# Kernel tuning notes

Hardware: AMD Instinct MI355X
Metric: run time of the kernel (lower is better)

The kernel has to match this reference:

```python
import jax, jax.numpy as jnp
import numpy as np

B, N, DOP, DM, H = 8, 2048, 256, 256, 256  # batch, n_ops==n_machines, dims


def setup_inputs() -> dict:
    key = jax.random.key(0)
    ks = jax.random.split(key, 21)
    s = 0.02
    inp = {
        "operation_features": jax.random.normal(ks[0], (B, N, DOP), jnp.float32),
        "machine_features": jax.random.normal(ks[1], (B, N, DM), jnp.float32),
        "type_match_mask": jax.random.bernoulli(ks[2], 0.3, (B, N, N)).astype(jnp.float32),
        "same_type_mask": jax.random.bernoulli(ks[3], 0.3, (B, N, N)).astype(jnp.float32),
        "oma_q_w": jax.random.normal(ks[4], (H, DM), jnp.float32) * s,
        "oma_q_b": jnp.zeros((H,), jnp.float32),
        "oma_kv_w": jax.random.normal(ks[5], (2 * H, DOP), jnp.float32) * s,
        "oma_kv_b": jnp.zeros((2 * H,), jnp.float32),
        "oma_s_w": jax.random.normal(ks[6], (1, 2 * H), jnp.float32) * s,
        "oma_s_b": jnp.zeros((1,), jnp.float32),
        "oma_o_w": jax.random.normal(ks[7], (DM, H), jnp.float32) * s,
        "oma_o_b": jnp.zeros((DM,), jnp.float32),
        "sa_w_w": jax.random.normal(ks[8], (3 * H, DM), jnp.float32) * s,
        "sa_w_b": jnp.zeros((3 * H,), jnp.float32),
        "sa_s_w": jax.random.normal(ks[9], (1, 2 * H), jnp.float32) * s,
        "sa_s_b": jnp.zeros((1,), jnp.float32),
        "sa_o_w": jax.random.normal(ks[10], (DM, H), jnp.float32) * s,
        "sa_o_b": jnp.zeros((DM,), jnp.float32),
        "mix_w": jax.random.normal(ks[11], (DM, 2 * DM), jnp.float32) * s,
        "mix_b": jnp.zeros((DM,), jnp.float32),
    }
    return inp


def reference(operation_features, machine_features, type_match_mask, same_type_mask,
              oma_q_w, oma_q_b, oma_kv_w, oma_kv_b, oma_s_w, oma_s_b, oma_o_w, oma_o_b,
              sa_w_w, sa_w_b, sa_s_w, sa_s_b, sa_o_w, sa_o_b, mix_w, mix_b):
    # --- OperationMachineAttention ---
    q = machine_features @ oma_q_w.T + oma_q_b            # (B,M,H)
    kv = operation_features @ oma_kv_w.T + oma_kv_b       # (B,C,2H)
    k, v = jnp.split(kv, 2, axis=-1)
    # Linear(cat([q,k])) == q @ W[:, :H].T + k @ W[:, H:].T + b (additive-score factorization)
    sq = jnp.einsum('bmh,h->bm', q, oma_s_w[0, :H])
    sk = jnp.einsum('bch,h->bc', k, oma_s_w[0, H:])
    scores = jax.nn.leaky_relu(sq[:, :, None] + sk[:, None, :] + oma_s_b[0])  # (B,M,C)
    p = jax.nn.softmax(scores * type_match_mask, axis=-1)
    wf = jnp.einsum('bmc,bch->bmh', p, v)
    operation_machine = wf @ oma_o_w.T + oma_o_b           # (B,M,DM)

    # --- SelfAttention over machines ---
    w3 = machine_features @ sa_w_w.T + sa_w_b              # (B,C,3H)
    q2, k2, v2 = jnp.split(w3, 3, axis=-1)
    sq2 = jnp.einsum('bih,h->bi', q2, sa_s_w[0, :H])
    sk2 = jnp.einsum('bjh,h->bj', k2, sa_s_w[0, H:])
    s2 = jax.nn.leaky_relu(sq2[:, :, None] + sk2[:, None, :] + sa_s_b[0])  # (B,C,C)
    p2 = jax.nn.softmax(s2 * same_type_mask, axis=-1)
    machine_machine = jnp.einsum('bij,bjh->bih', p2, v2) @ sa_o_w.T + sa_o_b  # (B,C,DM)

    # --- mix ---
    mixed = jnp.concatenate([operation_machine, machine_machine], axis=-1)
    return mixed @ mix_w.T + mix_b                          # (B,N,DM)
```

## Files before the change

### kernel.cpp

```cpp
#include <hip/hip_runtime.h>
#include <stdint.h>
#include <stddef.h>

#define B_ 8
#define N_ 2048
#define C_ 2048
#define D_ 256
#define H_ 256

typedef __bf16 bf16x8 __attribute__((ext_vector_type(8)));
typedef __bf16 bf16x4 __attribute__((ext_vector_type(4)));
typedef float f32x4 __attribute__((ext_vector_type(4)));

#define MFMA16(a, b, c) __builtin_amdgcn_mfma_f32_16x16x32_bf16((a), (b), (c), 0, 0, 0)

__global__ __launch_bounds__(256) void k0_vectors(
    const float* __restrict__ oma_q_w, const float* __restrict__ oma_q_b,
    const float* __restrict__ oma_kv_w, const float* __restrict__ oma_kv_b,
    const float* __restrict__ oma_s_w, const float* __restrict__ oma_s_b,
    const float* __restrict__ sa_w_w, const float* __restrict__ sa_w_b,
    const float* __restrict__ sa_s_w, const float* __restrict__ sa_s_b,
    float* __restrict__ wq_v, float* __restrict__ wk_v,
    float* __restrict__ wq2_v, float* __restrict__ wk2_v,
    float* __restrict__ sb)
{
    int d = threadIdx.x;
    float a0 = 0.f, a1 = 0.f, a2 = 0.f, a3 = 0.f;
    for (int h = 0; h < 256; ++h) {
        a0 += oma_q_w[h * 256 + d] * oma_s_w[h];
        a1 += oma_kv_w[h * 256 + d] * oma_s_w[256 + h];
        a2 += sa_w_w[h * 256 + d] * sa_s_w[h];
        a3 += sa_w_w[(256 + h) * 256 + d] * sa_s_w[256 + h];
    }
    wq_v[d] = a0; wk_v[d] = a1; wq2_v[d] = a2; wk2_v[d] = a3;

    int h = d;
    float p1 = oma_q_b[h] * oma_s_w[h] + oma_kv_b[h] * oma_s_w[256 + h];
    float p2 = sa_w_b[h] * sa_s_w[h] + sa_w_b[256 + h] * sa_s_w[256 + h];
    for (int o = 32; o; o >>= 1) { p1 += __shfl_xor(p1, o); p2 += __shfl_xor(p2, o); }
    __shared__ float redA[4], redB[4];
    int wv = threadIdx.x >> 6;
    if ((threadIdx.x & 63) == 0) { redA[wv] = p1; redB[wv] = p2; }
    __syncthreads();
    if (threadIdx.x == 0) {
        sb[0] = redA[0] + redA[1] + redA[2] + redA[3] + oma_s_b[0];
        sb[1] = redB[0] + redB[1] + redB[2] + redB[3] + sa_s_b[0];
    }
}

__global__ __launch_bounds__(256) void k1_wcat(
    const float* __restrict__ mix_w, const float* __restrict__ mix_b,
    const float* __restrict__ oma_o_w, const float* __restrict__ oma_o_b,
    const float* __restrict__ sa_o_w, const float* __restrict__ sa_o_b,
    __bf16* __restrict__ Wcat, float* __restrict__ b_total)
{
    int d = blockIdx.x, h = threadIdx.x;
    const float* mwr = mix_w + d * 512;
    float w1 = 0.f, w2 = 0.f;
    for (int e = 0; e < 256; ++e) {
        w1 += mwr[e] * oma_o_w[e * 256 + h];
        w2 += mwr[256 + e] * sa_o_w[e * 256 + h];
    }
    Wcat[d * 512 + h] = (__bf16)w1;
    Wcat[d * 512 + 256 + h] = (__bf16)w2;

    float pb = mwr[h] * oma_o_b[h] + mwr[256 + h] * sa_o_b[h];
    for (int o = 32; o; o >>= 1) pb += __shfl_xor(pb, o);
    __shared__ float red[4];
    if ((h & 63) == 0) red[h >> 6] = pb;
    __syncthreads();
    if (h == 0) b_total[d] = mix_b[d] + red[0] + red[1] + red[2] + red[3];
}

__global__ __launch_bounds__(256) void k2_scores(
    const float* __restrict__ op, const float* __restrict__ mach,
    const float* __restrict__ wq_v, const float* __restrict__ wk_v,
    const float* __restrict__ wq2_v, const float* __restrict__ wk2_v,
    const float* __restrict__ sb,
    float* __restrict__ sqp, float* __restrict__ skv,
    float* __restrict__ sq2p, float* __restrict__ sk2v)
{
    int t = threadIdx.x, lane = t & 63, wv = t >> 6;
    size_t n = (size_t)blockIdx.x * 4 + wv;
    const float4 mf = *(const float4*)(mach + n * 256 + lane * 4);
    const float4 of = *(const float4*)(op + n * 256 + lane * 4);
    const float4 q4 = *(const float4*)(wq_v + lane * 4);
    const float4 k4 = *(const float4*)(wk_v + lane * 4);
    const float4 q24 = *(const float4*)(wq2_v + lane * 4);
    const float4 k24 = *(const float4*)(wk2_v + lane * 4);
    float s1 = mf.x * q4.x + mf.y * q4.y + mf.z * q4.z + mf.w * q4.w;
    float s2 = of.x * k4.x + of.y * k4.y + of.z * k4.z + of.w * k4.w;
    float s3 = mf.x * q24.x + mf.y * q24.y + mf.z * q24.z + mf.w * q24.w;
    float s4 = mf.x * k24.x + mf.y * k24.y + mf.z * k24.z + mf.w * k24.w;
    for (int o = 32; o; o >>= 1) {
        s1 += __shfl_xor(s1, o); s2 += __shfl_xor(s2, o);
        s3 += __shfl_xor(s3, o); s4 += __shfl_xor(s4, o);
    }
    if (lane == 0) {
        sqp[n] = s1 + sb[0]; skv[n] = s2;
        sq2p[n] = s3 + sb[1]; sk2v[n] = s4;
    }
}

__global__ __launch_bounds__(256, 2) void k3_vgemm(
    const float* __restrict__ op, const float* __restrict__ mach,
    const float* __restrict__ oma_kv_w, const float* __restrict__ sa_w_w,
    __bf16* __restrict__ vt)
{
    __shared__ __attribute__((aligned(16))) __bf16 As[64][72];
    __shared__ __attribute__((aligned(16))) __bf16 Bs[64][72];
    int t = threadIdx.x;
    int bid = blockIdx.x;
    int which = bid >> 10;
    int r = bid & 1023;
    int b = r >> 7;
    int ht = (r >> 5) & 3;
    int ct = r & 31;

    const float* Aglob = (which ? (sa_w_w + 512 * 256) : (oma_kv_w + 256 * 256)) + ht * 64 * 256;
    const float* Bglob = (which ? mach : op) + ((size_t)b * N_ + ct * 64) * 256;

    int lane = t & 63, wv = t >> 6;
    int l15 = lane & 15, qo = (lane >> 4) * 8;
    int rr = t >> 4;
    int dd = (t & 15) * 4;

    f32x4 acc[4] = {};

    for (int d0 = 0; d0 < 256; d0 += 64) {
        #pragma unroll
        for (int p = 0; p < 4; ++p) {
            float4 av = *(const float4*)(Aglob + (size_t)(p * 16 + rr) * 256 + d0 + dd);
            float4 bv = *(const float4*)(Bglob + (size_t)(p * 16 + rr) * 256 + d0 + dd);
            bf16x4 a4, b4;
            a4[0] = (__bf16)av.x; a4[1] = (__bf16)av.y; a4[2] = (__bf16)av.z; a4[3] = (__bf16)av.w;
            b4[0] = (__bf16)bv.x; b4[1] = (__bf16)bv.y; b4[2] = (__bf16)bv.z; b4[3] = (__bf16)bv.w;
            *(bf16x4*)&As[p * 16 + rr][dd] = a4;
            *(bf16x4*)&Bs[p * 16 + rr][dd] = b4;
        }
        __syncthreads();
        #pragma unroll
        for (int kb = 0; kb < 2; ++kb) {
            bf16x8 bfr = *(const bf16x8*)&Bs[16 * wv + l15][kb * 32 + qo];
            #pragma unroll
            for (int rt = 0; rt < 4; ++rt) {
                bf16x8 afr = *(const bf16x8*)&As[16 * rt + l15][kb * 32 + qo];
                acc[rt] = MFMA16(afr, bfr, acc[rt]);
            }
        }
        __syncthreads();
    }
    #pragma unroll
    for (int rt = 0; rt < 4; ++rt)
        #pragma unroll
        for (int j = 0; j < 4; ++j)
            As[16 * rt + (lane >> 4) * 4 + j][16 * wv + l15] = (__bf16)acc[rt][j];
    __syncthreads();
    int hh = t >> 2, cb = (t & 3) * 16;
    __bf16* orow = vt + (((size_t)(which * 8 + b)) * 256 + ht * 64 + hh) * 2048 + ct * 64 + cb;
    *(bf16x8*)(orow) = *(const bf16x8*)&As[hh][cb];
    *(bf16x8*)(orow + 8) = *(const bf16x8*)&As[hh][cb + 8];
}

__global__ __launch_bounds__(256, 2) void k4_attn(
    const float* __restrict__ tmask, const float* __restrict__ smask,
    const float* __restrict__ sqp, const float* __restrict__ skv,
    const float* __restrict__ sq2p, const float* __restrict__ sk2v,
    const __bf16* __restrict__ vt,
    __bf16* __restrict__ wfcat)
{
    __shared__ __attribute__((aligned(16))) __bf16 eA[64][72];
    __shared__ __attribute__((aligned(16))) __bf16 vB[256][72];
    __shared__ float rowsum[64];

    int t = threadIdx.x;
    int bid = blockIdx.x;
    int which = bid >> 8;
    int r = bid & 255;
    int b = r >> 5;
    int m0 = (r & 31) * 64;

    const float* mask = (which ? smask : tmask) + ((size_t)b * N_ + m0) * C_;
    const float* sqrow = (which ? sq2p : sqp) + b * N_ + m0;
    const float* skrow = (which ? sk2v : skv) + b * N_;
    const __bf16* vbase = vt + ((size_t)(which * 8 + b)) * 256 * 2048;

    int lane = t & 63, wv = t >> 6;
    int l15 = lane & 15, qo = (lane >> 4) * 8;
    int mrow = t >> 2;
    int cqb = (t & 3) * 16;
    int vh = t >> 3;
    int vc = (t & 7) * 8;

    float sqv = sqrow[mrow];
    float psum = 0.f;
    f32x4 acc[4][4] = {};

    bf16x8 vv[8];
    float mk[16], skc[16];

    auto load_tiles = [&](int c0) {
        #pragma unroll
        for (int p = 0; p < 8; ++p)
            vv[p] = *(const bf16x8*)(vbase + (size_t)(p * 32 + vh) * 2048 + c0 + vc);
        #pragma unroll
        for (int i = 0; i < 4; ++i) {
            float4 m4 = *(const float4*)(mask + (size_t)mrow * C_ + c0 + cqb + i * 4);
            float4 s4 = *(const float4*)(skrow + c0 + cqb + i * 4);
            mk[4 * i + 0] = m4.x; mk[4 * i + 1] = m4.y; mk[4 * i + 2] = m4.z; mk[4 * i + 3] = m4.w;
            skc[4 * i + 0] = s4.x; skc[4 * i + 1] = s4.y; skc[4 * i + 2] = s4.z; skc[4 * i + 3] = s4.w;
        }
    };
    load_tiles(0);

    for (int c0 = 0; c0 < C_; c0 += 64) {
        #pragma unroll
        for (int p = 0; p < 8; ++p)
            *(bf16x8*)&vB[p * 32 + vh][vc] = vv[p];
        bf16x8 e0, e1;
        #pragma unroll
        for (int i = 0; i < 16; ++i) {
            float s = sqv + skc[i];
            s = s > 0.f ? s : 0.01f * s;
            float e = __expf(s * mk[i]);
            psum += e;
            if (i < 8) e0[i] = (__bf16)e; else e1[i - 8] = (__bf16)e;
        }
        *(bf16x8*)&eA[mrow][cqb] = e0;
        *(bf16x8*)&eA[mrow][cqb + 8] = e1;
        __syncthreads();
        int cn = c0 + 64; if (cn >= C_) cn = 0;
        load_tiles(cn);
        #pragma unroll
        for (int kb = 0; kb < 2; ++kb) {
            bf16x8 afr[4];
            #pragma unroll
            for (int rt = 0; rt < 4; ++rt)
                afr[rt] = *(const bf16x8*)&eA[16 * rt + l15][kb * 32 + qo];
            #pragma unroll
            for (int ctile = 0; ctile < 4; ++ctile) {
                bf16x8 bfr = *(const bf16x8*)&vB[64 * wv + 16 * ctile + l15][kb * 32 + qo];
                #pragma unroll
                for (int rt = 0; rt < 4; ++rt)
                    acc[rt][ctile] = MFMA16(afr[rt], bfr, acc[rt][ctile]);
            }
        }
        __syncthreads();
    }

    float rs = psum;
    rs += __shfl_xor(rs, 1);
    rs += __shfl_xor(rs, 2);
    if ((t & 3) == 0) rowsum[mrow] = rs;
    __syncthreads();

    __bf16* obuf = &vB[0][0];
    #pragma unroll
    for (int rt = 0; rt < 4; ++rt) {
        #pragma unroll
        for (int j = 0; j < 4; ++j) {
            int m = 16 * rt + (lane >> 4) * 4 + j;
            float inv = __builtin_amdgcn_rcpf(rowsum[m]);
            #pragma unroll
            for (int ctile = 0; ctile < 4; ++ctile)
                obuf[m * 264 + 64 * wv + 16 * ctile + l15] = (__bf16)(acc[rt][ctile][j] * inv);
        }
    }
    __syncthreads();
    int m = t >> 2, cb = (t & 3) * 64;
    __bf16* wrow = wfcat + ((size_t)(b * N_ + m0 + m)) * 512 + which * 256 + cb;
    #pragma unroll
    for (int k = 0; k < 8; ++k)
        *(bf16x8*)(wrow + k * 8) = *(const bf16x8*)&obuf[m * 264 + cb + k * 8];
}

__global__ __launch_bounds__(256, 2) void k5_out(
    const __bf16* __restrict__ wfcat, const __bf16* __restrict__ Wcat,
    const float* __restrict__ b_total, float* __restrict__ out)
{
    __shared__ __attribute__((aligned(16))) __bf16 As[64][72];
    __shared__ __attribute__((aligned(16))) __bf16 Bs[256][72];
    __shared__ float bias[256];
    int t = threadIdx.x;
    int n0 = blockIdx.x * 64;
    int lane = t & 63, wv = t >> 6, l15 = lane & 15, qo = (lane >> 4) * 8;
    bias[t] = b_total[t];
    int ar = t >> 3;
    int ac = (t & 7) * 8;
    f32x4 acc[4][4] = {};

    for (int k0 = 0; k0 < 512; k0 += 64) {
        #pragma unroll
        for (int p = 0; p < 2; ++p)
            *(bf16x8*)&As[p * 32 + ar][ac] =
                *(const bf16x8*)(wfcat + (size_t)(n0 + p * 32 + ar) * 512 + k0 + ac);
        #pragma unroll
        for (int p = 0; p < 8; ++p)
            *(bf16x8*)&Bs[p * 32 + ar][ac] =
                *(const bf16x8*)(Wcat + (size_t)(p * 32 + ar) * 512 + k0 + ac);
        __syncthreads();
        #pragma unroll
        for (int kb = 0; kb < 2; ++kb) {
            bf16x8 afr[4];
            #pragma unroll
            for (int rt = 0; rt < 4; ++rt)
                afr[rt] = *(const bf16x8*)&As[16 * rt + l15][kb * 32 + qo];
            #pragma unroll
            for (int ct = 0; ct < 4; ++ct) {
                bf16x8 bfr = *(const bf16x8*)&Bs[64 * wv + 16 * ct + l15][kb * 32 + qo];
                #pragma unroll
                for (int rt = 0; rt < 4; ++rt)
                    acc[rt][ct] = MFMA16(afr[rt], bfr, acc[rt][ct]);
            }
        }
        __syncthreads();
    }
    #pragma unroll
    for (int rt = 0; rt < 4; ++rt) {
        #pragma unroll
        for (int ct = 0; ct < 4; ++ct) {
            int d = 64 * wv + 16 * ct + l15;
            float bv = bias[d];
            #pragma unroll
            for (int j = 0; j < 4; ++j) {
                int m = 16 * rt + (lane >> 4) * 4 + j;
                out[(size_t)(n0 + m) * 256 + d] = acc[rt][ct][j] + bv;
            }
        }
    }
}

extern "C" void kernel_launch(void* const* d_in, const int* in_sizes, int n_in,
                              void* d_out, int out_size, void* d_ws, size_t ws_size,
                              hipStream_t stream)
{
    const float* op_feat  = (const float*)d_in[0];
    const float* mach_feat= (const float*)d_in[1];
    const float* tmask    = (const float*)d_in[2];
    const float* smask    = (const float*)d_in[3];
    const float* oma_q_w  = (const float*)d_in[4];
    const float* oma_q_b  = (const float*)d_in[5];
    const float* oma_kv_w = (const float*)d_in[6];
    const float* oma_kv_b = (const float*)d_in[7];
    const float* oma_s_w  = (const float*)d_in[8];
    const float* oma_s_b  = (const float*)d_in[9];
    const float* oma_o_w  = (const float*)d_in[10];
    const float* oma_o_b  = (const float*)d_in[11];
    const float* sa_w_w   = (const float*)d_in[12];
    const float* sa_w_b   = (const float*)d_in[13];
    const float* sa_s_w   = (const float*)d_in[14];
    const float* sa_s_b   = (const float*)d_in[15];
    const float* sa_o_w   = (const float*)d_in[16];
    const float* sa_o_b   = (const float*)d_in[17];
    const float* mix_w    = (const float*)d_in[18];
    const float* mix_b    = (const float*)d_in[19];

    char* ws = (char*)d_ws;
    float* wq_v   = (float*)(ws + 0);
    float* wk_v   = (float*)(ws + 1024);
    float* wq2_v  = (float*)(ws + 2048);
    float* wk2_v  = (float*)(ws + 3072);
    float* sb     = (float*)(ws + 4096);
    float* btot   = (float*)(ws + 4352);
    float* sqp    = (float*)(ws + 8192);
    float* skv    = (float*)(ws + 73728);
    float* sq2p   = (float*)(ws + 139264);
    float* sk2v   = (float*)(ws + 204800);
    __bf16* Wcat  = (__bf16*)(ws + 270336);
    __bf16* vt    = (__bf16*)(ws + 532480);
    __bf16* wfcat = (__bf16*)(ws + 17309696);
    float* outp   = (float*)d_out;

    k0_vectors<<<1, 256, 0, stream>>>(oma_q_w, oma_q_b, oma_kv_w, oma_kv_b,
                                      oma_s_w, oma_s_b, sa_w_w, sa_w_b,
                                      sa_s_w, sa_s_b, wq_v, wk_v, wq2_v, wk2_v, sb);
    k1_wcat<<<256, 256, 0, stream>>>(mix_w, mix_b, oma_o_w, oma_o_b,
                                     sa_o_w, sa_o_b, Wcat, btot);
    k2_scores<<<4096, 256, 0, stream>>>(op_feat, mach_feat, wq_v, wk_v, wq2_v, wk2_v,
                                        sb, sqp, skv, sq2p, sk2v);
    k3_vgemm<<<2048, 256, 0, stream>>>(op_feat, mach_feat, oma_kv_w, sa_w_w, vt);
    k4_attn<<<512, 256, 0, stream>>>(tmask, smask, sqp, skv, sq2p, sk2v, vt, wfcat);
    k5_out<<<256, 256, 0, stream>>>(wfcat, Wcat, btot, outp);
}
```

Baseline: 463.1 us.

## Restructure attention kernel with 32-row tiles, register-resident V and double-buffered scores

The attention kernel now processes 32 query rows per block with double-buffered exp tiles in LDS. V fragments are loaded directly from global memory into registers instead of being staged through shared memory, and mask loads are nontemporal. Block indices are swizzled across XCDs and occupancy is raised to four blocks per CU. The output GEMM is retiled to 32 rows, and the single-block vector reduction is split into a parallel partial pass plus a reduce. The aim is to overlap loads with MFMA work and raise parallelism, at the cost of redundant V reads from global/L2 per block.

```diff
diff --git a/kernel.cpp b/kernel.cpp
--- a/kernel.cpp
+++ b/kernel.cpp
@@ -14,23 +14,44 @@
 
 #define MFMA16(a, b, c) __builtin_amdgcn_mfma_f32_16x16x32_bf16((a), (b), (c), 0, 0, 0)
 
-__global__ __launch_bounds__(256) void k0_vectors(
-    const float* __restrict__ oma_q_w, const float* __restrict__ oma_q_b,
-    const float* __restrict__ oma_kv_w, const float* __restrict__ oma_kv_b,
+__global__ __launch_bounds__(256) void k0a_partial(
+    const float* __restrict__ oma_q_w, const float* __restrict__ oma_kv_w,
+    const float* __restrict__ sa_w_w,
+    const float* __restrict__ oma_s_w, const float* __restrict__ sa_s_w,
+    float* __restrict__ partial)
+{
+    int d = threadIdx.x;
+    int vec = blockIdx.x >> 3, hc = blockIdx.x & 7;
+    int h0 = hc * 32;
+    const float* Wb; const float* sv;
+    if (vec == 0)      { Wb = oma_q_w  + h0 * 256;         sv = oma_s_w + h0; }
+    else if (vec == 1) { Wb = oma_kv_w + h0 * 256;         sv = oma_s_w + 256 + h0; }
+    else if (vec == 2) { Wb = sa_w_w   + h0 * 256;         sv = sa_s_w + h0; }
+    else               { Wb = sa_w_w   + (256 + h0) * 256; sv = sa_s_w + 256 + h0; }
+    float a = 0.f;
+    #pragma unroll 8
+    for (int h = 0; h < 32; ++h) a += Wb[h * 256 + d] * sv[h];
+    partial[blockIdx.x * 256 + d] = a;
+}
+
+__global__ __launch_bounds__(256) void k0b_reduce(
+    const float* __restrict__ partial,
+    const float* __restrict__ oma_q_b, const float* __restrict__ oma_kv_b,
     const float* __restrict__ oma_s_w, const float* __restrict__ oma_s_b,
-    const float* __restrict__ sa_w_w, const float* __restrict__ sa_w_b,
-    const float* __restrict__ sa_s_w, const float* __restrict__ sa_s_b,
+    const float* __restrict__ sa_w_b, const float* __restrict__ sa_s_w,
+    const float* __restrict__ sa_s_b,
     float* __restrict__ wq_v, float* __restrict__ wk_v,
     float* __restrict__ wq2_v, float* __restrict__ wk2_v,
     float* __restrict__ sb)
 {
     int d = threadIdx.x;
     float a0 = 0.f, a1 = 0.f, a2 = 0.f, a3 = 0.f;
-    for (int h = 0; h < 256; ++h) {
-        a0 += oma_q_w[h * 256 + d] * oma_s_w[h];
-        a1 += oma_kv_w[h * 256 + d] * oma_s_w[256 + h];
-        a2 += sa_w_w[h * 256 + d] * sa_s_w[h];
-        a3 += sa_w_w[(256 + h) * 256 + d] * sa_s_w[256 + h];
+    #pragma unroll
+    for (int hc = 0; hc < 8; ++hc) {
+        a0 += partial[(0 * 8 + hc) * 256 + d];
+        a1 += partial[(1 * 8 + hc) * 256 + d];
+        a2 += partial[(2 * 8 + hc) * 256 + d];
+        a3 += partial[(3 * 8 + hc) * 256 + d];
     }
     wq_v[d] = a0; wk_v[d] = a1; wq2_v[d] = a2; wk2_v[d] = a3;
 
@@ -162,23 +183,29 @@
     *(bf16x8*)(orow + 8) = *(const bf16x8*)&As[hh][cb + 8];
 }
 
-__global__ __launch_bounds__(256, 2) void k4_attn(
+__device__ __forceinline__ f32x4 ntload4f(const float* p) {
+    return __builtin_nontemporal_load(reinterpret_cast<const f32x4*>(p));
+}
+
+__global__ __launch_bounds__(256, 4) void k4_attn(
     const float* __restrict__ tmask, const float* __restrict__ smask,
     const float* __restrict__ sqp, const float* __restrict__ skv,
     const float* __restrict__ sq2p, const float* __restrict__ sk2v,
     const __bf16* __restrict__ vt,
     __bf16* __restrict__ wfcat)
 {
-    __shared__ __attribute__((aligned(16))) __bf16 eA[64][72];
-    __shared__ __attribute__((aligned(16))) __bf16 vB[256][72];
-    __shared__ float rowsum[64];
+    __shared__ __attribute__((aligned(16))) __bf16 smem[32 * 264];
+    __shared__ float rowsum[32];
+    __bf16* eA0 = smem;
+    __bf16* eA1 = smem + 32 * 72;
 
     int t = threadIdx.x;
     int bid = blockIdx.x;
-    int which = bid >> 8;
-    int r = bid & 255;
-    int b = r >> 5;
-    int m0 = (r & 31) * 64;
+    int wg = (bid & 7) * 128 + (bid >> 3);
+    int which = wg >> 9;
+    int r = wg & 511;
+    int b = r >> 6;
+    int m0 = (r & 63) * 32;
 
     const float* mask = (which ? smask : tmask) + ((size_t)b * N_ + m0) * C_;
     const float* sqrow = (which ? sq2p : sqp) + b * N_ + m0;
@@ -187,90 +214,109 @@
 
     int lane = t & 63, wv = t >> 6;
     int l15 = lane & 15, qo = (lane >> 4) * 8;
-    int mrow = t >> 2;
-    int cqb = (t & 3) * 16;
-    int vh = t >> 3;
-    int vc = (t & 7) * 8;
+    int mrow = t >> 3;
+    int cq8 = (t & 7) * 8;
+
+    const __bf16* vptr = vbase + (size_t)(64 * wv + l15) * 2048 + qo;
+    const float* mrowp = mask + (size_t)mrow * C_ + cq8;
 
     float sqv = sqrow[mrow];
     float psum = 0.f;
-    f32x4 acc[4][4] = {};
-
-    bf16x8 vv[8];
-    float mk[16], skc[16];
-
-    auto load_tiles = [&](int c0) {
-        #pragma unroll
-        for (int p = 0; p < 8; ++p)
-            vv[p] = *(const bf16x8*)(vbase + (size_t)(p * 32 + vh) * 2048 + c0 + vc);
+    f32x4 acc[2][4] = {};
+
+    bf16x8 bfr[4][2];
+    float mkA[8], skA[8], mkB[8], skB[8];
+
+    auto load_ms = [&](int c0, float* mk, float* sk) {
+        f32x4 a = ntload4f(mrowp + c0);
+        f32x4 bq = ntload4f(mrowp + c0 + 4);
+        f32x4 s0 = *(const f32x4*)(skrow + c0 + cq8);
+        f32x4 s1 = *(const f32x4*)(skrow + c0 + cq8 + 4);
         #pragma unroll
         for (int i = 0; i < 4; ++i) {
-            float4 m4 = *(const float4*)(mask + (size_t)mrow * C_ + c0 + cqb + i * 4);
-            float4 s4 = *(const float4*)(skrow + c0 + cqb + i * 4);
-            mk[4 * i + 0] = m4.x; mk[4 * i + 1] = m4.y; mk[4 * i + 2] = m4.z; mk[4 * i + 3] = m4.w;
-            skc[4 * i + 0] = s4.x; skc[4 * i + 1] = s4.y; skc[4 * i + 2] = s4.z; skc[4 * i + 3] = s4.w;
+            mk[i] = a[i]; mk[4 + i] = bq[i];
+            sk[i] = s0[i]; sk[4 + i] = s1[i];
         }
     };
-    load_tiles(0);
-
-    for (int c0 = 0; c0 < C_; c0 += 64) {
-        #pragma unroll
-        for (int p = 0; p < 8; ++p)
-            *(bf16x8*)&vB[p * 32 + vh][vc] = vv[p];
-        bf16x8 e0, e1;
-        #pragma unroll
-        for (int i = 0; i < 16; ++i) {
-            float s = sqv + skc[i];
+    auto load_bfr = [&](int c0) {
+        #pragma unroll
+        for (int ct = 0; ct < 4; ++ct)
+            #pragma unroll
+            for (int kb = 0; kb < 2; ++kb)
+                bfr[ct][kb] = *(const bf16x8*)(vptr + (size_t)ct * 16 * 2048 + c0 + kb * 32);
+    };
+    auto compute_e = [&](const float* mk, const float* sk, __bf16* eb) {
+        bf16x8 ev;
+        #pragma unroll
+        for (int i = 0; i < 8; ++i) {
+            float s = sqv + sk[i];
             s = s > 0.f ? s : 0.01f * s;
             float e = __expf(s * mk[i]);
             psum += e;
-            if (i < 8) e0[i] = (__bf16)e; else e1[i - 8] = (__bf16)e;
-        }
-        *(bf16x8*)&eA[mrow][cqb] = e0;
-        *(bf16x8*)&eA[mrow][cqb + 8] = e1;
-        __syncthreads();
-        int cn = c0 + 64; if (cn >= C_) cn = 0;
-        load_tiles(cn);
+            ev[i] = (__bf16)e;
+        }
+        *(bf16x8*)&eb[mrow * 72 + cq8] = ev;
+    };
+    auto do_mfma = [&](const __bf16* eb) {
         #pragma unroll
         for (int kb = 0; kb < 2; ++kb) {
-            bf16x8 afr[4];
-            #pragma unroll
-            for (int rt = 0; rt < 4; ++rt)
-                afr[rt] = *(const bf16x8*)&eA[16 * rt + l15][kb * 32 + qo];
-            #pragma unroll
-            for (int ctile = 0; ctile < 4; ++ctile) {
-                bf16x8 bfr = *(const bf16x8*)&vB[64 * wv + 16 * ctile + l15][kb * 32 + qo];
-                #pragma unroll
-                for (int rt = 0; rt < 4; ++rt)
-                    acc[rt][ctile] = MFMA16(afr[rt], bfr, acc[rt][ctile]);
+            bf16x8 afr0 = *(const bf16x8*)&eb[l15 * 72 + kb * 32 + qo];
+            bf16x8 afr1 = *(const bf16x8*)&eb[(16 + l15) * 72 + kb * 32 + qo];
+            #pragma unroll
+            for (int ct = 0; ct < 4; ++ct) {
+                acc[0][ct] = MFMA16(afr0, bfr[ct][kb], acc[0][ct]);
+                acc[1][ct] = MFMA16(afr1, bfr[ct][kb], acc[1][ct]);
             }
         }
-        __syncthreads();
+    };
+
+    load_ms(0, mkA, skA);
+    load_ms(64, mkB, skB);
+    load_bfr(0);
+
+    #pragma unroll 1
+    for (int c0 = 0; c0 < C_; c0 += 128) {
+        compute_e(mkA, skA, eA0);
+        int cA = c0 + 128; if (cA >= C_) cA = 0;
+        load_ms(cA, mkA, skA);
+        asm volatile("s_waitcnt lgkmcnt(0)" ::: "memory");
+        __builtin_amdgcn_s_barrier();
+        do_mfma(eA0);
+        load_bfr(c0 + 64);
+        compute_e(mkB, skB, eA1);
+        int cB = c0 + 192; if (cB >= C_) cB = 0;
+        load_ms(cB, mkB, skB);
+        asm volatile("s_waitcnt lgkmcnt(0)" ::: "memory");
+        __builtin_amdgcn_s_barrier();
+        do_mfma(eA1);
+        int cN = c0 + 128; if (cN >= C_) cN = 0;
+        load_bfr(cN);
     }
 
     float rs = psum;
     rs += __shfl_xor(rs, 1);
     rs += __shfl_xor(rs, 2);
-    if ((t & 3) == 0) rowsum[mrow] = rs;
+    rs += __shfl_xor(rs, 4);
+    if ((t & 7) == 0) rowsum[mrow] = rs;
     __syncthreads();
 
-    __bf16* obuf = &vB[0][0];
+    __bf16* obuf = smem;
     #pragma unroll
-    for (int rt = 0; rt < 4; ++rt) {
+    for (int rt = 0; rt < 2; ++rt) {
         #pragma unroll
         for (int j = 0; j < 4; ++j) {
             int m = 16 * rt + (lane >> 4) * 4 + j;
             float inv = __builtin_amdgcn_rcpf(rowsum[m]);
             #pragma unroll
-            for (int ctile = 0; ctile < 4; ++ctile)
-                obuf[m * 264 + 64 * wv + 16 * ctile + l15] = (__bf16)(acc[rt][ctile][j] * inv);
+            for (int ct = 0; ct < 4; ++ct)
+                obuf[m * 264 + 64 * wv + 16 * ct + l15] = (__bf16)(acc[rt][ct][j] * inv);
         }
     }
     __syncthreads();
-    int m = t >> 2, cb = (t & 3) * 64;
+    int m = t >> 3, cb = (t & 7) * 32;
     __bf16* wrow = wfcat + ((size_t)(b * N_ + m0 + m)) * 512 + which * 256 + cb;
     #pragma unroll
-    for (int k = 0; k < 8; ++k)
+    for (int k = 0; k < 4; ++k)
         *(bf16x8*)(wrow + k * 8) = *(const bf16x8*)&obuf[m * 264 + cb + k * 8];
 }
 
@@ -278,22 +324,20 @@
     const __bf16* __restrict__ wfcat, const __bf16* __restrict__ Wcat,
     const float* __restrict__ b_total, float* __restrict__ out)
 {
-    __shared__ __attribute__((aligned(16))) __bf16 As[64][72];
+    __shared__ __attribute__((aligned(16))) __bf16 As[32][72];
     __shared__ __attribute__((aligned(16))) __bf16 Bs[256][72];
     __shared__ float bias[256];
     int t = threadIdx.x;
-    int n0 = blockIdx.x * 64;
+    int n0 = blockIdx.x * 32;
     int lane = t & 63, wv = t >> 6, l15 = lane & 15, qo = (lane >> 4) * 8;
     bias[t] = b_total[t];
     int ar = t >> 3;
     int ac = (t & 7) * 8;
-    f32x4 acc[4][4] = {};
+    f32x4 acc[2][4] = {};
 
     for (int k0 = 0; k0 < 512; k0 += 64) {
-        #pragma unroll
-        for (int p = 0; p < 2; ++p)
-            *(bf16x8*)&As[p * 32 + ar][ac] =
-                *(const bf16x8*)(wfcat + (size_t)(n0 + p * 32 + ar) * 512 + k0 + ac);
+        *(bf16x8*)&As[ar][ac] =
+            *(const bf16x8*)(wfcat + (size_t)(n0 + ar) * 512 + k0 + ac);
         #pragma unroll
         for (int p = 0; p < 8; ++p)
             *(bf16x8*)&Bs[p * 32 + ar][ac] =
@@ -301,22 +345,22 @@
         __syncthreads();
         #pragma unroll
         for (int kb = 0; kb < 2; ++kb) {
-            bf16x8 afr[4];
-            #pragma unroll
-            for (int rt = 0; rt < 4; ++rt)
+            bf16x8 afr[2];
+            #pragma unroll
+            for (int rt = 0; rt < 2; ++rt)
                 afr[rt] = *(const bf16x8*)&As[16 * rt + l15][kb * 32 + qo];
             #pragma unroll
             for (int ct = 0; ct < 4; ++ct) {
                 bf16x8 bfr = *(const bf16x8*)&Bs[64 * wv + 16 * ct + l15][kb * 32 + qo];
                 #pragma unroll
-                for (int rt = 0; rt < 4; ++rt)
+                for (int rt = 0; rt < 2; ++rt)
                     acc[rt][ct] = MFMA16(afr[rt], bfr, acc[rt][ct]);
             }
         }
         __syncthreads();
     }
     #pragma unroll
-    for (int rt = 0; rt < 4; ++rt) {
+    for (int rt = 0; rt < 2; ++rt) {
         #pragma unroll
         for (int ct = 0; ct < 4; ++ct) {
             int d = 64 * wv + 16 * ct + l15;
@@ -371,14 +415,18 @@
     __bf16* wfcat = (__bf16*)(ws + 17309696);
     float* outp   = (float*)d_out;
 
-    k0_vectors<<<1, 256, 0, stream>>>(oma_q_w, oma_q_b, oma_kv_w, oma_kv_b,
-                                      oma_s_w, oma_s_b, sa_w_w, sa_w_b,
-                                      sa_s_w, sa_s_b, wq_v, wk_v, wq2_v, wk2_v, sb);
+    float* partial = (float*)(ws + 532480);
+
+    k0a_partial<<<32, 256, 0, stream>>>(oma_q_w, oma_kv_w, sa_w_w,
+                                        oma_s_w, sa_s_w, partial);
+    k0b_reduce<<<1, 256, 0, stream>>>(partial, oma_q_b, oma_kv_b, oma_s_w, oma_s_b,
+                                      sa_w_b, sa_s_w, sa_s_b,
+                                      wq_v, wk_v, wq2_v, wk2_v, sb);
     k1_wcat<<<256, 256, 0, stream>>>(mix_w, mix_b, oma_o_w, oma_o_b,
                                      sa_o_w, sa_o_b, Wcat, btot);
     k2_scores<<<4096, 256, 0, stream>>>(op_feat, mach_feat, wq_v, wk_v, wq2_v, wk2_v,
                                         sb, sqp, skv, sq2p, sk2v);
     k3_vgemm<<<2048, 256, 0, stream>>>(op_feat, mach_feat, oma_kv_w, sa_w_w, vt);
-    k4_attn<<<512, 256, 0, stream>>>(tmask, smask, sqp, skv, sq2p, sk2v, vt, wfcat);
-    k5_out<<<256, 256, 0, stream>>>(wfcat, Wcat, btot, outp);
-}
+    k4_attn<<<1024, 256, 0, stream>>>(tmask, smask, sqp, skv, sq2p, sk2v, vt, wfcat);
+    k5_out<<<512, 256, 0, stream>>>(wfcat, Wcat, btot, outp);
+}
```

Measured after the change: 475.5 us. 1.03x slower.
